# Performance work log

Measured on AMD Instinct MI355X. Metric: run time of the kernel, lower is better.

Reference implementation:

```python
import jax, jax.numpy as jnp
import numpy as np

SEQ_LEN = 512
DIM = 256
HEADS = 8
DIM_HEAD = 32
INNER = HEADS * DIM_HEAD
BATCH = 1
LN_EPS = 1e-5


def setup_inputs() -> dict:
    key = jax.random.key(0)
    ks = jax.random.split(key, 6)
    # kaiming_uniform_(a=sqrt(5)) on [L, in, out] -> bound = 1/sqrt(fan_in) with fan_in = in_dim*out_dim? 
    # torch computes fan_in from dims [1:] => fan_in = in_dim (dim of -2) * ... in practice bound ~ sqrt(1/fan_in);
    # exact init distribution is irrelevant for correctness testing, use uniform(+-1/sqrt(DIM)).
    s = 1.0 / np.sqrt(DIM)
    so = 1.0 / np.sqrt(INNER)
    return {
        "x": jax.random.normal(ks[0], (BATCH, SEQ_LEN, DIM), jnp.float32),
        "Wq": jax.random.uniform(ks[1], (SEQ_LEN, DIM, INNER), jnp.float32, -s, s),
        "Wk": jax.random.uniform(ks[2], (SEQ_LEN, DIM, INNER), jnp.float32, -s, s),
        "Wv": jax.random.uniform(ks[3], (SEQ_LEN, DIM, INNER), jnp.float32, -s, s),
        "gamma": jnp.ones((DIM,), jnp.float32),
        "beta": jnp.zeros((DIM,), jnp.float32),
        "Wo": jax.random.uniform(ks[4], (INNER, DIM), jnp.float32, -so, so),
        "bo": jnp.zeros((DIM,), jnp.float32),
    }


def reference(x, Wq, Wk, Wv, gamma, beta, Wo, bo):
    b, n, dim = x.shape
    h, dh = HEADS, DIM_HEAD
    # LayerNorm
    mu = jnp.mean(x, axis=-1, keepdims=True)
    var = jnp.mean((x - mu) ** 2, axis=-1, keepdims=True)
    xn = (x - mu) / jnp.sqrt(var + LN_EPS) * gamma + beta
    # Per-relative-index projections: pd[b, r, m, e] = xn[b, m] @ W[r]
    qd = jnp.einsum('bmc,rce->brme', xn, Wq)
    kd = jnp.einsum('bmc,rce->brme', xn, Wk)
    vd = jnp.einsum('bmc,rce->brme', xn, Wv)
    i = jnp.arange(n)
    # to_q / to_v index map: max(0, i - j); to_k (after rearrange swap) uses min(0, m - n) + n - 1
    rq = jnp.maximum(0, i[:, None] - i[None, :])          # [n(query), m(key)]
    rk = jnp.minimum(0, i[None, :] - i[:, None]) + n - 1  # [n, m]
    # q[b,n,m,e] = qd[b, rq[n,m], m]; k[b,n,m,e] = kd[b, rk[n,m], n]; v like q
    q_full = qd[:, rq, i[None, :], :].reshape(b, n, n, h, dh)
    k_full = kd[:, rk, i[:, None], :].reshape(b, n, n, h, dh)
    v_full = vd[:, rq, i[None, :], :].reshape(b, n, n, h, dh)
    scale = dh ** -0.5
    dots = jnp.einsum('bnmhd,bnmhd->bhnm', q_full, k_full) * scale
    causal = i[:, None] >= i[None, :]  # tril
    dots = jnp.where(causal[None, None], dots, -jnp.inf)
    attn = jax.nn.softmax(dots, axis=-1)
    out = jnp.einsum('bhnm,bnmhd->bnhd', attn, v_full).reshape(b, n, h * dh)
    return out @ Wo + bo
```

## Files before the change

### kernel.cpp

```cpp
#include <hip/hip_runtime.h>
#include <hip/hip_bf16.h>

typedef unsigned short u16;
typedef unsigned int   u32;
typedef __bf16 bf16x8 __attribute__((ext_vector_type(8)));
typedef float  f32x4  __attribute__((ext_vector_type(4)));
typedef u32    u32x4  __attribute__((ext_vector_type(4)));
typedef u32    u32x2  __attribute__((ext_vector_type(2)));

#define TRI_TOTAL 131328

__device__ __forceinline__ float b2f(u16 u) {
    return __builtin_bit_cast(float, ((u32)u) << 16);
}
__device__ __forceinline__ u16 f2b(float f) {
    return __builtin_bit_cast(u16, __float2bfloat16(f));
}
__device__ __forceinline__ int pcol(int col) {
    return (((col & 7) ^ ((col >> 3) & 7)) << 4);
}
__device__ __forceinline__ void gload_lds16(const void* g, void* l) {
    __builtin_amdgcn_global_load_lds(
        (const __attribute__((address_space(1))) void*)g,
        (__attribute__((address_space(3))) void*)l, 16, 0, 0);
}

__global__ void __launch_bounds__(256) ln_kernel(const float* __restrict__ x,
                                                 const float* __restrict__ g,
                                                 const float* __restrict__ b,
                                                 u16* __restrict__ xn) {
    int n = blockIdx.x, t = threadIdx.x;
    float v = x[n * 256 + t];
    __shared__ float red[4];
    float s = v;
    #pragma unroll
    for (int o = 32; o >= 1; o >>= 1) s += __shfl_xor(s, o);
    if ((t & 63) == 0) red[t >> 6] = s;
    __syncthreads();
    float mu = (red[0] + red[1] + red[2] + red[3]) * (1.0f / 256.0f);
    float d = v - mu;
    __syncthreads();
    float s2 = d * d;
    #pragma unroll
    for (int o = 32; o >= 1; o >>= 1) s2 += __shfl_xor(s2, o);
    if ((t & 63) == 0) red[t >> 6] = s2;
    __syncthreads();
    float var = (red[0] + red[1] + red[2] + red[3]) * (1.0f / 256.0f);
    float y = d * rsqrtf(var + 1e-5f) * g[t] + b[t];
    xn[n * 256 + t] = f2b(y);
}

__global__ void __launch_bounds__(256) proj_kernel(
        const u16* __restrict__ xn,
        const float* __restrict__ Wq, const float* __restrict__ Wk,
        const float* __restrict__ Wv,
        u16* __restrict__ Qa, u16* __restrict__ Ka, u16* __restrict__ Va) {
    __shared__ char lds[65536 + 64 * 144];
    char* bufA = lds;
    char* bufB = lds + 32768;
    char* obuf = lds + 65536;

    int bid = blockIdx.x;
    int which = bid % 3;
    int rr = bid / 3;
    int strip = rr >> 2;
    int cs = rr & 3;
    const float* W = (which == 0) ? Wq : ((which == 1) ? Wk : Wv);
    u16* Out       = (which == 0) ? Qa : ((which == 1) ? Ka : Va);

    int t = threadIdx.x;
    int c0 = cs * 64;
    int wv  = t >> 6;
    int rg  = wv >> 1;
    int cg  = wv & 1;
    int L   = t & 63;
    int l15 = L & 15, l4 = L >> 4;
    int c4 = (t & 15) * 4;
    int kq = t >> 4;

    int r, rows, pbase, nbase;
#define SET_R(Q) do {                                                         \
    int rq_ = strip * 4 + (Q);                                                \
    r = (which == 1) ? (511 - rq_) : rq_;                                     \
    rows  = (which == 1) ? (r + 1) : (512 - r);                               \
    pbase = (which == 1) ? (511 - r) : 0;                                     \
    nbase = (which == 1) ? (511 - r) : 0 + r;                                 \
    if (which == 1) nbase = 511 - r;                                          \
} while (0)
    SET_R(0);

#define DMA_TILE(DST, M0) do {                                                \
    _Pragma("unroll")                                                         \
    for (int j = 0; j < 8; ++j) {                                             \
        int lrow = wv * 16 + 2 * j + (L >> 5);                                \
        int grow = pbase + (M0) + lrow; if (grow > 511) grow = 511;           \
        const char* gp = (const char*)xn + (size_t)grow * 512                 \
                         + (((L & 31) ^ (lrow & 7)) << 4);                    \
        char* lp = (DST) + (wv * 16 + 2 * j) * 512;                           \
        gload_lds16(gp, lp);                                                  \
    }                                                                         \
} while (0)

#define DMA_WHALF(DST, R) do {                                                \
    const char* wsrc = (const char*)(W + ((size_t)(R) << 16) + c0);           \
    _Pragma("unroll")                                                         \
    for (int p = 0; p < 8; ++p) {                                             \
        int kk = p * 16 + (t >> 4);                                           \
        const char* gp = wsrc + (size_t)kk * 1024 + (t & 15) * 16;            \
        char* lp = (DST) + p * 4096 + (t >> 6) * 1024;                        \
        gload_lds16(gp, lp);                                                  \
    }                                                                         \
} while (0)

#define WLW(DST, IT, VA, VB, VC, VD) {                                        \
        int kbase2 = (kq * 4 + (IT) * 64) * 2;                                \
        _Pragma("unroll")                                                     \
        for (int i = 0; i < 4; ++i) {                                         \
            int col = c4 + i;                                                 \
            u32 lo = (u32)f2b(VA[i]) | ((u32)f2b(VB[i]) << 16);               \
            u32 hi = (u32)f2b(VC[i]) | ((u32)f2b(VD[i]) << 16);               \
            u32x2 pr; pr[0] = lo; pr[1] = hi;                                 \
            *(u32x2*)((DST) + col * 512 + (kbase2 ^ pcol(col))) = pr;         \
        }                                                                     \
    }

    DMA_TILE(bufB, 0);

    {
        const float* wp = W + ((size_t)r << 16) + c0 + c4 + (size_t)(kq * 4) * 256;
        f32x4 w00 = *(const f32x4*)(wp + 0);
        f32x4 w01 = *(const f32x4*)(wp + 256);
        f32x4 w02 = *(const f32x4*)(wp + 512);
        f32x4 w03 = *(const f32x4*)(wp + 768);
        f32x4 w10 = *(const f32x4*)(wp + 16384 + 0);
        f32x4 w11 = *(const f32x4*)(wp + 16384 + 256);
        f32x4 w12 = *(const f32x4*)(wp + 16384 + 512);
        f32x4 w13 = *(const f32x4*)(wp + 16384 + 768);
        f32x4 w20 = *(const f32x4*)(wp + 32768 + 0);
        f32x4 w21 = *(const f32x4*)(wp + 32768 + 256);
        f32x4 w22 = *(const f32x4*)(wp + 32768 + 512);
        f32x4 w23 = *(const f32x4*)(wp + 32768 + 768);
        f32x4 w30 = *(const f32x4*)(wp + 49152 + 0);
        f32x4 w31 = *(const f32x4*)(wp + 49152 + 256);
        f32x4 w32 = *(const f32x4*)(wp + 49152 + 512);
        f32x4 w33 = *(const f32x4*)(wp + 49152 + 768);
        WLW(bufA, 0, w00, w01, w02, w03)
        WLW(bufA, 1, w10, w11, w12, w13)
        WLW(bufA, 2, w20, w21, w22, w23)
        WLW(bufA, 3, w30, w31, w32, w33)
    }
    __syncthreads();

    bf16x8 b00, b01, b02, b03, b04, b05, b06, b07;
    bf16x8 b10, b11, b12, b13, b14, b15, b16, b17;
#define BEXT(SRC) do {                                                        \
    int colA_ = cg * 32 + l15, colB_ = cg * 32 + 16 + l15;                    \
    b00 = *(const bf16x8*)((SRC) + colA_ * 512 + ((0*64 + l4*16) ^ pcol(colA_))); \
    b01 = *(const bf16x8*)((SRC) + colA_ * 512 + ((1*64 + l4*16) ^ pcol(colA_))); \
    b02 = *(const bf16x8*)((SRC) + colA_ * 512 + ((2*64 + l4*16) ^ pcol(colA_))); \
    b03 = *(const bf16x8*)((SRC) + colA_ * 512 + ((3*64 + l4*16) ^ pcol(colA_))); \
    b04 = *(const bf16x8*)((SRC) + colA_ * 512 + ((4*64 + l4*16) ^ pcol(colA_))); \
    b05 = *(const bf16x8*)((SRC) + colA_ * 512 + ((5*64 + l4*16) ^ pcol(colA_))); \
    b06 = *(const bf16x8*)((SRC) + colA_ * 512 + ((6*64 + l4*16) ^ pcol(colA_))); \
    b07 = *(const bf16x8*)((SRC) + colA_ * 512 + ((7*64 + l4*16) ^ pcol(colA_))); \
    b10 = *(const bf16x8*)((SRC) + colB_ * 512 + ((0*64 + l4*16) ^ pcol(colB_))); \
    b11 = *(const bf16x8*)((SRC) + colB_ * 512 + ((1*64 + l4*16) ^ pcol(colB_))); \
    b12 = *(const bf16x8*)((SRC) + colB_ * 512 + ((2*64 + l4*16) ^ pcol(colB_))); \
    b13 = *(const bf16x8*)((SRC) + colB_ * 512 + ((3*64 + l4*16) ^ pcol(colB_))); \
    b14 = *(const bf16x8*)((SRC) + colB_ * 512 + ((4*64 + l4*16) ^ pcol(colB_))); \
    b15 = *(const bf16x8*)((SRC) + colB_ * 512 + ((5*64 + l4*16) ^ pcol(colB_))); \
    b16 = *(const bf16x8*)((SRC) + colB_ * 512 + ((6*64 + l4*16) ^ pcol(colB_))); \
    b17 = *(const bf16x8*)((SRC) + colB_ * 512 + ((7*64 + l4*16) ^ pcol(colB_))); \
} while (0)
    BEXT(bufA);
    __syncthreads();

    int am = (l15 & 7) << 4;
    char* cur = bufB;
    char* alt = bufA;
    int tr = t >> 2, qd = t & 3;

    for (int q = 0;;) {
        int rnext = 0;
        if (q < 3) { int rq_ = strip * 4 + q + 1;
                     rnext = (which == 1) ? (511 - rq_) : rq_; }
        int nt = (rows + 63) >> 6;
        for (int i = 0; i < nt; ++i) {
            int m0 = i << 6;
            bool lastt = (i + 1 >= nt);
            if (!lastt)          DMA_TILE(alt, m0 + 64);
            else if (q < 3)      DMA_WHALF(alt, rnext);

            const char* abase = cur + (rg * 32 + l15) * 512;
            f32x4 acc00 = {}, acc01 = {}, acc10 = {}, acc11 = {};
#define KS(ks) {                                                              \
        int kb = (ks) * 64 + l4 * 16;                                         \
        bf16x8 a0 = *(const bf16x8*)(abase + (kb ^ am));                      \
        bf16x8 a1 = *(const bf16x8*)(abase + 16 * 512 + (kb ^ am));           \
        acc00 = __builtin_amdgcn_mfma_f32_16x16x32_bf16(a0, b0##ks, acc00, 0, 0, 0); \
        acc01 = __builtin_amdgcn_mfma_f32_16x16x32_bf16(a0, b1##ks, acc01, 0, 0, 0); \
        acc10 = __builtin_amdgcn_mfma_f32_16x16x32_bf16(a1, b0##ks, acc10, 0, 0, 0); \
        acc11 = __builtin_amdgcn_mfma_f32_16x16x32_bf16(a1, b1##ks, acc11, 0, 0, 0); \
    }
            KS(0) KS(1) KS(2) KS(3) KS(4) KS(5) KS(6) KS(7)
#undef KS
            {
                char* ob = obuf + (size_t)(rg * 32) * 144 + (cg * 32 + l15) * 2;
                #pragma unroll
                for (int rf = 0; rf < 2; ++rf) {
                    f32x4 va = rf ? acc10 : acc00;
                    f32x4 vb = rf ? acc11 : acc01;
                    #pragma unroll
                    for (int j = 0; j < 4; ++j) {
                        int rl = rf * 16 + l4 * 4 + j;
                        *(u16*)(ob + rl * 144)      = f2b(va[j]);
                        *(u16*)(ob + rl * 144 + 32) = f2b(vb[j]);
                    }
                }
            }
            __syncthreads();
            {
                int ml = m0 + tr;
                if (ml < rows) {
                    u32 nout = (u32)(nbase + ml);
                    u32 prow = (nout * (nout + 1)) >> 1;
                    u16* op = Out + (size_t)(prow + (u32)ml) * 256 + c0 + qd * 16;
                    const char* lb = obuf + tr * 144 + qd * 32;
                    u32x4 o0 = *(const u32x4*)(lb);
                    u32x4 o1 = *(const u32x4*)(lb + 16);
                    *(u32x4*)op = o0;
                    *(u32x4*)(op + 8) = o1;
                }
            }
            if (!lastt) { asm volatile("s_waitcnt vmcnt(2)" ::: "memory"); }
            else        { asm volatile("s_waitcnt vmcnt(0)" ::: "memory"); }
            __builtin_amdgcn_s_barrier();
            __builtin_amdgcn_sched_barrier(0);
            { char* tmp = cur; cur = alt; alt = tmp; }
        }
        if (++q > 3) break;
        SET_R(q);
        DMA_TILE(alt, 0);
        const float* wpg = W + ((size_t)r << 16) + c0 + c4;
        f32x4 gw0 = *(const f32x4*)(wpg + 32768 + (size_t)(kq * 4 + 0) * 256);
        f32x4 gw1 = *(const f32x4*)(wpg + 32768 + (size_t)(kq * 4 + 1) * 256);
        f32x4 gw2 = *(const f32x4*)(wpg + 32768 + (size_t)(kq * 4 + 2) * 256);
        f32x4 gw3 = *(const f32x4*)(wpg + 32768 + (size_t)(kq * 4 + 3) * 256);
        f32x4 gw4 = *(const f32x4*)(wpg + 49152 + (size_t)(kq * 4 + 0) * 256);
        f32x4 gw5 = *(const f32x4*)(wpg + 49152 + (size_t)(kq * 4 + 1) * 256);
        f32x4 gw6 = *(const f32x4*)(wpg + 49152 + (size_t)(kq * 4 + 2) * 256);
        f32x4 gw7 = *(const f32x4*)(wpg + 49152 + (size_t)(kq * 4 + 3) * 256);
        f32x4 lw0 = *(const f32x4*)(cur + (kq * 4 + 0) * 256 + (t & 15) * 16);
        f32x4 lw1 = *(const f32x4*)(cur + (kq * 4 + 1) * 256 + (t & 15) * 16);
        f32x4 lw2 = *(const f32x4*)(cur + (kq * 4 + 2) * 256 + (t & 15) * 16);
        f32x4 lw3 = *(const f32x4*)(cur + (kq * 4 + 3) * 256 + (t & 15) * 16);
        f32x4 lw4 = *(const f32x4*)(cur + (64 + kq * 4 + 0) * 256 + (t & 15) * 16);
        f32x4 lw5 = *(const f32x4*)(cur + (64 + kq * 4 + 1) * 256 + (t & 15) * 16);
        f32x4 lw6 = *(const f32x4*)(cur + (64 + kq * 4 + 2) * 256 + (t & 15) * 16);
        f32x4 lw7 = *(const f32x4*)(cur + (64 + kq * 4 + 3) * 256 + (t & 15) * 16);
        __syncthreads();
        WLW(cur, 0, lw0, lw1, lw2, lw3)
        WLW(cur, 1, lw4, lw5, lw6, lw7)
        WLW(cur, 2, gw0, gw1, gw2, gw3)
        WLW(cur, 3, gw4, gw5, gw6, gw7)
        asm volatile("s_waitcnt vmcnt(0)" ::: "memory");
        __syncthreads();
        BEXT(cur);
        __syncthreads();
        { char* tmp = cur; cur = alt; alt = tmp; }
    }
#undef DMA_TILE
#undef DMA_WHALF
#undef WLW
#undef BEXT
#undef SET_R
}

__global__ void __launch_bounds__(256) attn_kernel(const u16* __restrict__ Qa,
                                                   const u16* __restrict__ Ka,
                                                   const u16* __restrict__ Va,
                                                   float* __restrict__ ao) {
    int n = 511 - blockIdx.x, t = threadIdx.x;
    __shared__ float pbuf[512 * 9];
    __shared__ float linv[8];
    int band = n + 1;
    size_t rb = (size_t)(n * (n + 1) / 2);

    int h = t & 7, mi = t >> 3;
    for (int m0 = 0; m0 < band; m0 += 32) {
        int m = m0 + mi;
        float d = -1e30f;
        if (m < band) {
            const char* qp = (const char*)Qa + (rb + m) * 512 + h * 64;
            const char* kp = (const char*)Ka + (rb + m) * 512 + h * 64;
            float acc = 0.f;
            #pragma unroll
            for (int cch = 0; cch < 4; ++cch) {
                u32x4 qv = *reinterpret_cast<const u32x4*>(qp + cch * 16);
                u32x4 kv = *reinterpret_cast<const u32x4*>(kp + cch * 16);
                #pragma unroll
                for (int i = 0; i < 4; ++i) {
                    float ql = __builtin_bit_cast(float, qv[i] << 16);
                    float qh = __builtin_bit_cast(float, qv[i] & 0xffff0000u);
                    float kl = __builtin_bit_cast(float, kv[i] << 16);
                    float kh = __builtin_bit_cast(float, kv[i] & 0xffff0000u);
                    acc += ql * kl + qh * kh;
                }
            }
            d = acc * 0.17677669529663687f;
        }
        pbuf[m * 9 + h] = d;
    }
    __syncthreads();

    int wv = t >> 6, L = t & 63;
    for (int s = 0; s < 2; ++s) {
        int hh = wv + s * 4;
        float mx = -1e30f;
        for (int m = L; m < band; m += 64) mx = fmaxf(mx, pbuf[m * 9 + hh]);
        #pragma unroll
        for (int o = 32; o >= 1; o >>= 1) mx = fmaxf(mx, __shfl_xor(mx, o));
        float sum = 0.f;
        for (int m = L; m < band; m += 64) {
            float p = __expf(pbuf[m * 9 + hh] - mx);
            pbuf[m * 9 + hh] = p;
            sum += p;
        }
        #pragma unroll
        for (int o = 32; o >= 1; o >>= 1) sum += __shfl_xor(sum, o);
        if (L == 0) linv[hh] = 1.0f / sum;
    }
    __syncthreads();

    int h2 = t >> 5;
    const char* vp = (const char*)Va + rb * 512 + (size_t)t * 2;
    const float* pb = pbuf + h2;
    float a0 = 0, a1 = 0, a2 = 0, a3 = 0, a4 = 0, a5 = 0, a6 = 0, a7 = 0;
    int m = 0;
    for (; m + 16 <= band; m += 16) {
        u16 v0  = *(const u16*)(vp + (size_t)(m +  0) * 512);
        u16 v1  = *(const u16*)(vp + (size_t)(m +  1) * 512);
        u16 v2  = *(const u16*)(vp + (size_t)(m +  2) * 512);
        u16 v3  = *(const u16*)(vp + (size_t)(m +  3) * 512);
        u16 v4  = *(const u16*)(vp + (size_t)(m +  4) * 512);
        u16 v5  = *(const u16*)(vp + (size_t)(m +  5) * 512);
        u16 v6  = *(const u16*)(vp + (size_t)(m +  6) * 512);
        u16 v7  = *(const u16*)(vp + (size_t)(m +  7) * 512);
        u16 v8  = *(const u16*)(vp + (size_t)(m +  8) * 512);
        u16 v9  = *(const u16*)(vp + (size_t)(m +  9) * 512);
        u16 v10 = *(const u16*)(vp + (size_t)(m + 10) * 512);
        u16 v11 = *(const u16*)(vp + (size_t)(m + 11) * 512);
        u16 v12 = *(const u16*)(vp + (size_t)(m + 12) * 512);
        u16 v13 = *(const u16*)(vp + (size_t)(m + 13) * 512);
        u16 v14 = *(const u16*)(vp + (size_t)(m + 14) * 512);
        u16 v15 = *(const u16*)(vp + (size_t)(m + 15) * 512);
        a0 += pb[(m +  0) * 9] * b2f(v0);
        a1 += pb[(m +  1) * 9] * b2f(v1);
        a2 += pb[(m +  2) * 9] * b2f(v2);
        a3 += pb[(m +  3) * 9] * b2f(v3);
        a4 += pb[(m +  4) * 9] * b2f(v4);
        a5 += pb[(m +  5) * 9] * b2f(v5);
        a6 += pb[(m +  6) * 9] * b2f(v6);
        a7 += pb[(m +  7) * 9] * b2f(v7);
        a0 += pb[(m +  8) * 9] * b2f(v8);
        a1 += pb[(m +  9) * 9] * b2f(v9);
        a2 += pb[(m + 10) * 9] * b2f(v10);
        a3 += pb[(m + 11) * 9] * b2f(v11);
        a4 += pb[(m + 12) * 9] * b2f(v12);
        a5 += pb[(m + 13) * 9] * b2f(v13);
        a6 += pb[(m + 14) * 9] * b2f(v14);
        a7 += pb[(m + 15) * 9] * b2f(v15);
    }
    for (; m < band; ++m)
        a0 += pb[m * 9] * b2f(*(const u16*)(vp + (size_t)m * 512));
    ao[n * 256 + t] = (((a0 + a1) + (a2 + a3)) + ((a4 + a5) + (a6 + a7)))
                      * linv[h2];
}

__global__ void __launch_bounds__(256) outproj_kernel(const float* __restrict__ ao,
                                                      const float* __restrict__ Wo,
                                                      const float* __restrict__ bo,
                                                      float* __restrict__ out) {
    int n = blockIdx.x, e = threadIdx.x;
    const float* a = ao + n * 256;
    float c0 = bo[e], c1 = 0, c2 = 0, c3 = 0;
    for (int c = 0; c < 256; c += 4) {
        c0 += a[c + 0] * Wo[(c + 0) * 256 + e];
        c1 += a[c + 1] * Wo[(c + 1) * 256 + e];
        c2 += a[c + 2] * Wo[(c + 2) * 256 + e];
        c3 += a[c + 3] * Wo[(c + 3) * 256 + e];
    }
    out[n * 256 + e] = (c0 + c1) + (c2 + c3);
}

extern "C" void kernel_launch(void* const* d_in, const int* in_sizes, int n_in,
                              void* d_out, int out_size, void* d_ws, size_t ws_size,
                              hipStream_t stream) {
    const float* x     = (const float*)d_in[0];
    const float* Wq    = (const float*)d_in[1];
    const float* Wk    = (const float*)d_in[2];
    const float* Wv    = (const float*)d_in[3];
    const float* gamma = (const float*)d_in[4];
    const float* beta  = (const float*)d_in[5];
    const float* Wo    = (const float*)d_in[6];
    const float* bo    = (const float*)d_in[7];
    float* out = (float*)d_out;

    char* ws = (char*)d_ws;
    u16* xn = (u16*)ws;
    size_t off = (size_t)512 * 256 * 2;
    u16* Qa = (u16*)(ws + off); off += (size_t)TRI_TOTAL * 256 * 2;
    u16* Ka = (u16*)(ws + off); off += (size_t)TRI_TOTAL * 256 * 2;
    u16* Va = (u16*)(ws + off); off += (size_t)TRI_TOTAL * 256 * 2;
    float* ao = (float*)(ws + off);

    ln_kernel<<<512, 256, 0, stream>>>(x, gamma, beta, xn);
    proj_kernel<<<1536, 256, 0, stream>>>(xn, Wq, Wk, Wv, Qa, Ka, Va);
    attn_kernel<<<512, 256, 0, stream>>>(Qa, Ka, Va, ao);
    outproj_kernel<<<512, 256, 0, stream>>>(ao, Wo, bo, out);
}
```

Before: 231.4 us.

## Store projected Q/K/V grouped by relative index instead of by query row

The projection kernel now writes each weight slice's output rows contiguously in one block (offset by qoff/koff of the relative index) rather than scattering them into the query-row triangular layout. The writes become long contiguous runs, which should help store coalescing in the projection kernel. In exchange, the attention kernel gathers Q, K and V rows from scattered locations with per-row index arithmetic, and the V loop unroll drops from 16 to 8, so its reads lose locality.

```diff
diff --git a/kernel.cpp b/kernel.cpp
--- a/kernel.cpp
+++ b/kernel.cpp
@@ -23,6 +23,12 @@
     __builtin_amdgcn_global_load_lds(
         (const __attribute__((address_space(1))) void*)g,
         (__attribute__((address_space(3))) void*)l, 16, 0, 0);
+}
+__device__ __forceinline__ u32 qoff(int d) {
+    return 512u * (u32)d - (u32)((d * (d - 1)) >> 1);
+}
+__device__ __forceinline__ u32 koff(int r) {
+    return (u32)((r * (r + 1)) >> 1);
 }
 
 __global__ void __launch_bounds__(256) ln_kernel(const float* __restrict__ x,
@@ -78,14 +84,14 @@
     int c4 = (t & 15) * 4;
     int kq = t >> 4;
 
-    int r, rows, pbase, nbase;
+    int r, rows, pbase;
+    u32 obase;
 #define SET_R(Q) do {                                                         \
     int rq_ = strip * 4 + (Q);                                                \
     r = (which == 1) ? (511 - rq_) : rq_;                                     \
     rows  = (which == 1) ? (r + 1) : (512 - r);                               \
     pbase = (which == 1) ? (511 - r) : 0;                                     \
-    nbase = (which == 1) ? (511 - r) : 0 + r;                                 \
-    if (which == 1) nbase = 511 - r;                                          \
+    obase = (which == 1) ? koff(r) : qoff(r);                                 \
 } while (0)
     SET_R(0);
 
@@ -222,9 +228,7 @@
             {
                 int ml = m0 + tr;
                 if (ml < rows) {
-                    u32 nout = (u32)(nbase + ml);
-                    u32 prow = (nout * (nout + 1)) >> 1;
-                    u16* op = Out + (size_t)(prow + (u32)ml) * 256 + c0 + qd * 16;
+                    u16* op = Out + (size_t)(obase + (u32)ml) * 256 + c0 + qd * 16;
                     const char* lb = obuf + tr * 144 + qd * 32;
                     u32x4 o0 = *(const u32x4*)(lb);
                     u32x4 o1 = *(const u32x4*)(lb + 16);
@@ -284,15 +288,17 @@
     __shared__ float pbuf[512 * 9];
     __shared__ float linv[8];
     int band = n + 1;
-    size_t rb = (size_t)(n * (n + 1) / 2);
 
     int h = t & 7, mi = t >> 3;
     for (int m0 = 0; m0 < band; m0 += 32) {
         int m = m0 + mi;
         float d = -1e30f;
         if (m < band) {
-            const char* qp = (const char*)Qa + (rb + m) * 512 + h * 64;
-            const char* kp = (const char*)Ka + (rb + m) * 512 + h * 64;
+            int dd = n - m;
+            u32 qrow = qoff(dd) + (u32)m;
+            u32 krow = koff(511 - dd) + (u32)m;
+            const char* qp = (const char*)Qa + (size_t)qrow * 512 + h * 64;
+            const char* kp = (const char*)Ka + (size_t)krow * 512 + h * 64;
             float acc = 0.f;
             #pragma unroll
             for (int cch = 0; cch < 4; ++cch) {
@@ -333,46 +339,32 @@
     __syncthreads();
 
     int h2 = t >> 5;
-    const char* vp = (const char*)Va + rb * 512 + (size_t)t * 2;
+    const char* vb = (const char*)Va + (size_t)t * 2;
     const float* pb = pbuf + h2;
     float a0 = 0, a1 = 0, a2 = 0, a3 = 0, a4 = 0, a5 = 0, a6 = 0, a7 = 0;
     int m = 0;
-    for (; m + 16 <= band; m += 16) {
-        u16 v0  = *(const u16*)(vp + (size_t)(m +  0) * 512);
-        u16 v1  = *(const u16*)(vp + (size_t)(m +  1) * 512);
-        u16 v2  = *(const u16*)(vp + (size_t)(m +  2) * 512);
-        u16 v3  = *(const u16*)(vp + (size_t)(m +  3) * 512);
-        u16 v4  = *(const u16*)(vp + (size_t)(m +  4) * 512);
-        u16 v5  = *(const u16*)(vp + (size_t)(m +  5) * 512);
-        u16 v6  = *(const u16*)(vp + (size_t)(m +  6) * 512);
-        u16 v7  = *(const u16*)(vp + (size_t)(m +  7) * 512);
-        u16 v8  = *(const u16*)(vp + (size_t)(m +  8) * 512);
-        u16 v9  = *(const u16*)(vp + (size_t)(m +  9) * 512);
-        u16 v10 = *(const u16*)(vp + (size_t)(m + 10) * 512);
-        u16 v11 = *(const u16*)(vp + (size_t)(m + 11) * 512);
-        u16 v12 = *(const u16*)(vp + (size_t)(m + 12) * 512);
-        u16 v13 = *(const u16*)(vp + (size_t)(m + 13) * 512);
-        u16 v14 = *(const u16*)(vp + (size_t)(m + 14) * 512);
-        u16 v15 = *(const u16*)(vp + (size_t)(m + 15) * 512);
-        a0 += pb[(m +  0) * 9] * b2f(v0);
-        a1 += pb[(m +  1) * 9] * b2f(v1);
-        a2 += pb[(m +  2) * 9] * b2f(v2);
-        a3 += pb[(m +  3) * 9] * b2f(v3);
-        a4 += pb[(m +  4) * 9] * b2f(v4);
-        a5 += pb[(m +  5) * 9] * b2f(v5);
-        a6 += pb[(m +  6) * 9] * b2f(v6);
-        a7 += pb[(m +  7) * 9] * b2f(v7);
-        a0 += pb[(m +  8) * 9] * b2f(v8);
-        a1 += pb[(m +  9) * 9] * b2f(v9);
-        a2 += pb[(m + 10) * 9] * b2f(v10);
-        a3 += pb[(m + 11) * 9] * b2f(v11);
-        a4 += pb[(m + 12) * 9] * b2f(v12);
-        a5 += pb[(m + 13) * 9] * b2f(v13);
-        a6 += pb[(m + 14) * 9] * b2f(v14);
-        a7 += pb[(m + 15) * 9] * b2f(v15);
+#define VROW(MM) ((size_t)(qoff(n - (MM)) + (u32)(MM)) * 512)
+    for (; m + 8 <= band; m += 8) {
+        u16 v0 = *(const u16*)(vb + VROW(m + 0));
+        u16 v1 = *(const u16*)(vb + VROW(m + 1));
+        u16 v2 = *(const u16*)(vb + VROW(m + 2));
+        u16 v3 = *(const u16*)(vb + VROW(m + 3));
+        u16 v4 = *(const u16*)(vb + VROW(m + 4));
+        u16 v5 = *(const u16*)(vb + VROW(m + 5));
+        u16 v6 = *(const u16*)(vb + VROW(m + 6));
+        u16 v7 = *(const u16*)(vb + VROW(m + 7));
+        a0 += pb[(m + 0) * 9] * b2f(v0);
+        a1 += pb[(m + 1) * 9] * b2f(v1);
+        a2 += pb[(m + 2) * 9] * b2f(v2);
+        a3 += pb[(m + 3) * 9] * b2f(v3);
+        a4 += pb[(m + 4) * 9] * b2f(v4);
+        a5 += pb[(m + 5) * 9] * b2f(v5);
+        a6 += pb[(m + 6) * 9] * b2f(v6);
+        a7 += pb[(m + 7) * 9] * b2f(v7);
     }
     for (; m < band; ++m)
-        a0 += pb[m * 9] * b2f(*(const u16*)(vp + (size_t)m * 512));
+        a0 += pb[m * 9] * b2f(*(const u16*)(vb + VROW(m)));
+#undef VROW
     ao[n * 256 + t] = (((a0 + a1) + (a2 + a3)) + ((a4 + a5) + (a6 + a7)))
                       * linv[h2];
 }
```

Result: slower. 241.8 us (+4.5%).
